# Performance work log

Measured on AMD Instinct MI355X. Metric: run time of the kernel, lower is better.

Reference implementation:

```python
import jax, jax.numpy as jnp
import numpy as np

N, DIM, NINC = 2_000_000, 8, 1000


def setup_inputs() -> dict:
    key = jax.random.key(0)
    k_u, k_w = jax.random.split(key)
    u = jax.random.uniform(k_u, (N, DIM), dtype=jnp.float32)
    # Non-uniform but monotone grid per dim over [0, 1]: cumulative of positive random increments.
    w = jax.random.uniform(k_w, (DIM, NINC), dtype=jnp.float32) + 0.5
    cdf = jnp.cumsum(w, axis=1) / jnp.sum(w, axis=1, keepdims=True)  # [dim, ninc], ends at 1
    grid = jnp.concatenate([jnp.zeros((DIM, 1), jnp.float32), cdf], axis=1)  # [dim, ninc+1]
    inc = grid[:, 1:] - grid[:, :-1]  # [dim, ninc]
    return {"u": u, "grid": grid, "inc": inc, "ninc": NINC}


def reference(u, grid, inc, ninc):
    # u: [N, dim]; grid: [dim, ninc+1]; inc: [dim, ninc]
    u_ninc = u * ninc
    iu = jnp.floor(u_ninc).astype(jnp.int32)        # [N, dim] bin index
    du = u_ninc - iu                                 # fractional part within bin
    mask = iu < ninc                                 # points exactly at / beyond upper edge
    iu_c = jnp.clip(iu, 0, ninc - 1)
    # Gather per-dim grid lower edge and increment at each point's bin: [N, dim]
    g = jnp.take_along_axis(grid, iu_c.T, axis=1).T
    h = jnp.take_along_axis(inc, iu_c.T, axis=1).T
    upper = grid[:, ninc][None, :]                   # [1, dim]
    inc_last = inc[:, ninc - 1][None, :]             # [1, dim]
    x = jnp.where(mask, g + h * du, upper)
    fac = jnp.where(mask, h, inc_last) * ninc        # per-dim Jacobian factor
    log_jac = jnp.sum(jnp.log(fac), axis=1)          # [N]
    return x, log_jac
```

## Files before the change

### kernel.cpp

```cpp
#include <hip/hip_runtime.h>

#define TPB 256
#define NDIM 8

__global__ __launch_bounds__(TPB) void vegas_map_kernel(
    const float* __restrict__ u,
    const float* __restrict__ grid,
    float* __restrict__ x_out,
    float* __restrict__ lj_out,
    int n, int gcols)
{
    extern __shared__ float lds_grid[];
    const int ninc = gcols - 1;
    const int gtot = NDIM * gcols;

    for (int t = threadIdx.x; t < gtot; t += TPB)
        lds_grid[t] = grid[t];
    __syncthreads();

    const float fninc = (float)ninc;
    const float4* __restrict__ u4 = (const float4*)u;
    float4* __restrict__ x4 = (float4*)x_out;

    const int stride = gridDim.x * TPB;
    for (int p = blockIdx.x * TPB + threadIdx.x; p < n; p += stride) {
        float4 ua = u4[2 * p];
        float4 ub = u4[2 * p + 1];
        float uv[NDIM] = {ua.x, ua.y, ua.z, ua.w, ub.x, ub.y, ub.z, ub.w};
        float xv[NDIM];
        float prod = 1.0f;

        #pragma unroll
        for (int d = 0; d < NDIM; ++d) {
            float un = uv[d] * fninc;
            int   iu = (int)un;
            float du = un - (float)iu;
            bool  in = iu < ninc;
            int   iuc = in ? iu : (ninc - 1);
            const float* row = lds_grid + d * gcols;
            float g0 = row[iuc];
            float g1 = row[iuc + 1];
            float h  = g1 - g0;
            xv[d] = in ? (g0 + h * du) : row[ninc];
            prod *= h * fninc;
        }

        float4 oa = {xv[0], xv[1], xv[2], xv[3]};
        float4 ob = {xv[4], xv[5], xv[6], xv[7]};
        x4[2 * p]     = oa;
        x4[2 * p + 1] = ob;
        lj_out[p] = logf(prod);
    }
}

extern "C" void kernel_launch(void* const* d_in, const int* in_sizes, int n_in,
                              void* d_out, int out_size, void* d_ws, size_t ws_size,
                              hipStream_t stream) {
    const float* u    = (const float*)d_in[0];
    const float* grid = (const float*)d_in[1];
    const int n     = in_sizes[0] / NDIM;
    const int gcols = in_sizes[1] / NDIM;

    float* x_out  = (float*)d_out;
    float* lj_out = (float*)d_out + (size_t)n * NDIM;

    int blocks = (n + TPB - 1) / TPB;
    if (blocks > 2048) blocks = 2048;
    size_t lds_bytes = (size_t)NDIM * gcols * sizeof(float);

    vegas_map_kernel<<<blocks, TPB, lds_bytes, stream>>>(u, grid, x_out, lj_out, n, gcols);
}
```

Before: 31.66 us.

## Use nontemporal loads/stores, process two points per thread, vectorize LDS fill

Switches global loads and stores of u, x and log-jacobian to nontemporal builtins, and makes each thread handle two strided points per iteration so more loads are in flight. The grid copy into LDS uses 4-wide vectors, block size grows to 512 with an occupancy hint, and the grid is capped at 1024 blocks. The aim is better memory-level parallelism and less cache pollution on a bandwidth-bound streaming kernel, at the cost of more registers per thread. The 4-wide LDS fill assumes NDIM*gcols is a multiple of four, which holds here (8*1001).

```diff
diff --git a/kernel.cpp b/kernel.cpp
--- a/kernel.cpp
+++ b/kernel.cpp
@@ -1,9 +1,11 @@
 #include <hip/hip_runtime.h>
 
-#define TPB 256
+#define TPB 512
 #define NDIM 8
 
-__global__ __launch_bounds__(TPB) void vegas_map_kernel(
+typedef float fvec4 __attribute__((ext_vector_type(4)));
+
+__global__ __launch_bounds__(TPB, 8) void vegas_map_kernel(
     const float* __restrict__ u,
     const float* __restrict__ grid,
     float* __restrict__ x_out,
@@ -12,44 +14,68 @@
 {
     extern __shared__ float lds_grid[];
     const int ninc = gcols - 1;
-    const int gtot = NDIM * gcols;
+    const int gtot4 = (NDIM * gcols) >> 2;
 
-    for (int t = threadIdx.x; t < gtot; t += TPB)
-        lds_grid[t] = grid[t];
+    const fvec4* __restrict__ g4 = (const fvec4*)grid;
+    fvec4* lds4 = (fvec4*)lds_grid;
+    for (int t = threadIdx.x; t < gtot4; t += TPB)
+        lds4[t] = g4[t];
     __syncthreads();
 
     const float fninc = (float)ninc;
-    const float4* __restrict__ u4 = (const float4*)u;
-    float4* __restrict__ x4 = (float4*)x_out;
+    const fvec4* __restrict__ u4 = (const fvec4*)u;
+    fvec4* __restrict__ x4 = (fvec4*)x_out;
 
     const int stride = gridDim.x * TPB;
-    for (int p = blockIdx.x * TPB + threadIdx.x; p < n; p += stride) {
-        float4 ua = u4[2 * p];
-        float4 ub = u4[2 * p + 1];
-        float uv[NDIM] = {ua.x, ua.y, ua.z, ua.w, ub.x, ub.y, ub.z, ub.w};
-        float xv[NDIM];
-        float prod = 1.0f;
+
+    for (int p = blockIdx.x * TPB + threadIdx.x; p < n; p += 2 * stride) {
+        const int q = p + stride;
+        const bool hq = (q < n);
+
+        fvec4 a0 = __builtin_nontemporal_load(u4 + 2 * p);
+        fvec4 b0 = __builtin_nontemporal_load(u4 + 2 * p + 1);
+        fvec4 a1 = a0, b1 = b0;
+        if (hq) {
+            a1 = __builtin_nontemporal_load(u4 + 2 * q);
+            b1 = __builtin_nontemporal_load(u4 + 2 * q + 1);
+        }
 
         #pragma unroll
-        for (int d = 0; d < NDIM; ++d) {
-            float un = uv[d] * fninc;
-            int   iu = (int)un;
-            float du = un - (float)iu;
-            bool  in = iu < ninc;
-            int   iuc = in ? iu : (ninc - 1);
-            const float* row = lds_grid + d * gcols;
-            float g0 = row[iuc];
-            float g1 = row[iuc + 1];
-            float h  = g1 - g0;
-            xv[d] = in ? (g0 + h * du) : row[ninc];
-            prod *= h * fninc;
+        for (int pt = 0; pt < 2; ++pt) {
+            if (pt == 1 && !hq) break;
+            const int idx = (pt == 0) ? p : q;
+            float uv[NDIM];
+            if (pt == 0) {
+                uv[0]=a0.x; uv[1]=a0.y; uv[2]=a0.z; uv[3]=a0.w;
+                uv[4]=b0.x; uv[5]=b0.y; uv[6]=b0.z; uv[7]=b0.w;
+            } else {
+                uv[0]=a1.x; uv[1]=a1.y; uv[2]=a1.z; uv[3]=a1.w;
+                uv[4]=b1.x; uv[5]=b1.y; uv[6]=b1.z; uv[7]=b1.w;
+            }
+
+            float xv[NDIM];
+            float prod = 1.0f;
+            #pragma unroll
+            for (int d = 0; d < NDIM; ++d) {
+                float un = uv[d] * fninc;
+                int   iu = (int)un;
+                float du = un - (float)iu;
+                bool  in = iu < ninc;
+                int   iuc = in ? iu : (ninc - 1);
+                const float* row = lds_grid + d * gcols;
+                float g0 = row[iuc];
+                float g1 = row[iuc + 1];
+                float h  = g1 - g0;
+                xv[d] = in ? (g0 + h * du) : row[ninc];
+                prod *= h * fninc;
+            }
+
+            fvec4 oa = {xv[0], xv[1], xv[2], xv[3]};
+            fvec4 ob = {xv[4], xv[5], xv[6], xv[7]};
+            __builtin_nontemporal_store(oa, x4 + 2 * idx);
+            __builtin_nontemporal_store(ob, x4 + 2 * idx + 1);
+            __builtin_nontemporal_store(logf(prod), lj_out + idx);
         }
-
-        float4 oa = {xv[0], xv[1], xv[2], xv[3]};
-        float4 ob = {xv[4], xv[5], xv[6], xv[7]};
-        x4[2 * p]     = oa;
-        x4[2 * p + 1] = ob;
-        lj_out[p] = logf(prod);
     }
 }
 
@@ -65,7 +91,7 @@
     float* lj_out = (float*)d_out + (size_t)n * NDIM;
 
     int blocks = (n + TPB - 1) / TPB;
-    if (blocks > 2048) blocks = 2048;
+    if (blocks > 1024) blocks = 1024;
     size_t lds_bytes = (size_t)NDIM * gcols * sizeof(float);
 
     vegas_map_kernel<<<blocks, TPB, lds_bytes, stream>>>(u, grid, x_out, lj_out, n, gcols);
```

Result: slower. 33.99 us (+7.4%).
